# Kernel tuning notes

Measured on AMD Instinct MI355X. Metric: run time of the kernel, lower is better.

## Reference

```python
import math
import jax, jax.numpy as jnp
import numpy as np

B, L, C, H = 2, 2048, 1024, 16
D = C // H


def new_gelu(x):
    return 0.5 * x * (1.0 + jnp.tanh(math.sqrt(2.0 / math.pi) * (x + 0.044715 * x ** 3)))


def layer_norm(x, w, b, eps=1e-5):
    mu = jnp.mean(x, axis=-1, keepdims=True)
    var = jnp.var(x, axis=-1, keepdims=True)
    return (x - mu) * jax.lax.rsqrt(var + eps) * w + b


def setup_inputs() -> dict:
    key = jax.random.key(0)
    ks = jax.random.split(key, 8)
    s = 0.02
    return {
        "x": jax.random.normal(ks[0], (B, L, C), dtype=jnp.float32),
        "ln1_w": jnp.ones((C,), jnp.float32),
        "ln1_b": jnp.zeros((C,), jnp.float32),
        "w_attn": jax.random.normal(ks[1], (C, 3 * C), dtype=jnp.float32) * s,
        "b_attn": jnp.zeros((3 * C,), jnp.float32),
        "w_proj": jax.random.normal(ks[2], (C, C), dtype=jnp.float32) * s,
        "b_proj": jnp.zeros((C,), jnp.float32),
        "ln2_w": jnp.ones((C,), jnp.float32),
        "ln2_b": jnp.zeros((C,), jnp.float32),
        "w_fc": jax.random.normal(ks[3], (C, 4 * C), dtype=jnp.float32) * s,
        "b_fc": jnp.zeros((4 * C,), jnp.float32),
        "w_fc2": jax.random.normal(ks[4], (4 * C, C), dtype=jnp.float32) * s,
        "b_fc2": jnp.zeros((C,), jnp.float32),
    }


def reference(x, ln1_w, ln1_b, w_attn, b_attn, w_proj, b_proj,
              ln2_w, ln2_b, w_fc, b_fc, w_fc2, b_fc2):
    # --- self-attention sublayer (pre-LN) ---
    h = layer_norm(x, ln1_w, ln1_b)
    qkv = h @ w_attn + b_attn                              # [B, L, 3C]
    q, k, v = jnp.split(qkv, 3, axis=-1)
    q = q.reshape(B, L, H, D)
    k = k.reshape(B, L, H, D)
    v = v.reshape(B, L, H, D)
    att = jnp.einsum("bqhd,bkhd->bhqk", q, k) * (1.0 / math.sqrt(D))
    causal = jnp.tril(jnp.ones((L, L), dtype=bool))
    att = jnp.where(causal[None, None], att, -jnp.inf)
    att = jax.nn.softmax(att, axis=-1)
    y = jnp.einsum("bhqk,bkhd->bqhd", att, v).reshape(B, L, C)
    y = y @ w_proj + b_proj
    x = x + y
    # --- MLP sublayer (pre-LN) ---
    h = layer_norm(x, ln2_w, ln2_b)
    h = new_gelu(h @ w_fc + b_fc)
    h = h @ w_fc2 + b_fc2
    return x + h
```

## Files before the change

### kernel.cpp

```cpp
#include <hip/hip_runtime.h>
#include <math.h>

#define B_ 2
#define L_ 2048
#define C_ 1024
#define H_ 16
#define M_ (B_*L_)

typedef short s16x8 __attribute__((ext_vector_type(8)));
typedef float f32x4 __attribute__((ext_vector_type(4)));

__device__ __forceinline__ unsigned short f2bf(float f) {
    unsigned int u = __float_as_uint(f);
    u += 0x7fffu + ((u >> 16) & 1u);
    return (unsigned short)(u >> 16);
}

__device__ __forceinline__ void gl_lds16(const void* g, void* l) {
    __builtin_amdgcn_global_load_lds(
        (const __attribute__((address_space(1))) void*)g,
        (__attribute__((address_space(3))) void*)l, 16, 0, 0);
}

__device__ __forceinline__ void ln_row(const float* __restrict__ x,
                                       const float* __restrict__ w,
                                       const float* __restrict__ b,
                                       unsigned short* __restrict__ out,
                                       int row, int t,
                                       float* red0, float* red1, float* mv) {
    float4 v = ((const float4*)(x + (size_t)row * C_))[t];
    float s  = v.x + v.y + v.z + v.w;
    float s2 = v.x*v.x + v.y*v.y + v.z*v.z + v.w*v.w;
    #pragma unroll
    for (int off = 32; off > 0; off >>= 1) {
        s  += __shfl_down(s, off);
        s2 += __shfl_down(s2, off);
    }
    int wave = t >> 6, lane = t & 63;
    if (lane == 0) { red0[wave] = s; red1[wave] = s2; }
    __syncthreads();
    if (t == 0) {
        float a = red0[0] + red0[1] + red0[2] + red0[3];
        float c = red1[0] + red1[1] + red1[2] + red1[3];
        float mean = a * (1.0f / C_);
        mv[0] = mean;
        mv[1] = rsqrtf(c * (1.0f / C_) - mean * mean + 1e-5f);
    }
    __syncthreads();
    float mean = mv[0], rstd = mv[1];
    float4 wv = ((const float4*)w)[t];
    float4 bv = ((const float4*)b)[t];
    ushort4 o;
    o.x = f2bf((v.x - mean) * rstd * wv.x + bv.x);
    o.y = f2bf((v.y - mean) * rstd * wv.y + bv.y);
    o.z = f2bf((v.z - mean) * rstd * wv.z + bv.z);
    o.w = f2bf((v.w - mean) * rstd * wv.w + bv.w);
    *(ushort4*)&out[(size_t)row * C_ + t * 4] = o;
}

__global__ __launch_bounds__(256) void ln_bf16(const float* __restrict__ x,
                                               const float* __restrict__ w,
                                               const float* __restrict__ b,
                                               unsigned short* __restrict__ out) {
    __shared__ float red0[4], red1[4], mv[2];
    ln_row(x, w, b, out, blockIdx.x, threadIdx.x, red0, red1, mv);
}

__global__ __launch_bounds__(256) void prep_kernel(
    const float* __restrict__ W0, unsigned short* __restrict__ T0,
    const float* __restrict__ W1, unsigned short* __restrict__ T1,
    const float* __restrict__ W2, unsigned short* __restrict__ T2,
    const float* __restrict__ W3, unsigned short* __restrict__ T3,
    const float* __restrict__ x, const float* __restrict__ lnw,
    const float* __restrict__ lnb, unsigned short* __restrict__ h) {
    __shared__ unsigned short Ts[32][33];
    __shared__ float red0[4], red1[4], mv[2];
    int id = blockIdx.x;
    int t = threadIdx.x;
    if (id >= 12288) {
        ln_row(x, lnw, lnb, h, id - 12288, t, red0, red1, mv);
        return;
    }
    const float* W; unsigned short* WT; int R, C, bx, by;
    if (id < 3072)      { W = W0; WT = T0; R = 1024; C = 3072; bx = id % 96;  by = id / 96; }
    else if (id < 4096) { W = W1; WT = T1; R = 1024; C = 1024; id -= 3072; bx = id & 31;  by = id >> 5; }
    else if (id < 8192) { W = W2; WT = T2; R = 1024; C = 4096; id -= 4096; bx = id & 127; by = id >> 7; }
    else                { W = W3; WT = T3; R = 4096; C = 1024; id -= 8192; bx = id & 31;  by = id >> 5; }
    int tx = t & 31, ty = t >> 5;
    int c0 = bx * 32, r0 = by * 32;
    #pragma unroll
    for (int k = 0; k < 4; ++k)
        Ts[ty + 8*k][tx] = f2bf(W[(size_t)(r0 + ty + 8*k) * C + c0 + tx]);
    __syncthreads();
    #pragma unroll
    for (int k = 0; k < 4; ++k)
        WT[(size_t)(c0 + ty + 8*k) * R + r0 + tx] = Ts[tx][ty + 8*k];
}

__global__ __launch_bounds__(256) void transpose_v(const unsigned short* __restrict__ qkv,
                                                   unsigned short* __restrict__ Vt) {
    __shared__ unsigned short Ts[32][33];
    int t = threadIdx.x;
    int tx = t & 31, ty = t >> 5;
    int by = blockIdx.y;
    int bh = by >> 1, dt = by & 1;
    int b = bh >> 4, h = bh & 15;
    int l0 = blockIdx.x * 32, d0 = dt * 32;
    #pragma unroll
    for (int k = 0; k < 4; ++k)
        Ts[ty + 8*k][tx] = qkv[(size_t)(b * L_ + l0 + ty + 8*k) * (3*C_) + 2*C_ + h*64 + d0 + tx];
    __syncthreads();
    #pragma unroll
    for (int k = 0; k < 4; ++k)
        Vt[(size_t)(bh*64 + d0 + ty + 8*k) * L_ + l0 + tx] = Ts[tx][ty + 8*k];
}

__device__ __forceinline__ float gelu_f(float x) {
    float u2 = 1.5957691216057308f * (x + 0.044715f * x * x * x);
    return x / (1.0f + __expf(-u2));
}

template<int ACT, int OBF, int TN, int SC, int KS>
__global__ __launch_bounds__(256) void bgemm(const unsigned short* __restrict__ A,
                                             const unsigned short* __restrict__ BT,
                                             const float* __restrict__ bias,
                                             const float* __restrict__ res,
                                             void* __restrict__ Cout,
                                             int M, int N, int K) {
    __shared__ __align__(16) unsigned short As[128 * 64];
    __shared__ __align__(16) unsigned short Bs[TN * 64];
    const int t = threadIdx.x, w = t >> 6, quad = (t & 63) >> 4, ln15 = t & 15;
    constexpr int FJ = TN / 32;
    const int woff_m = (w >> 1) * 64, woff_n = (w & 1) * (TN / 2);
    const int m0g = blockIdx.y * 128, n0g = blockIdx.x * TN;
    f32x4 acc[4][FJ];
    #pragma unroll
    for (int fi = 0; fi < 4; ++fi)
        #pragma unroll
        for (int fj = 0; fj < FJ; ++fj)
            #pragma unroll
            for (int i = 0; i < 4; ++i) acc[fi][fj][i] = 0.0f;

    const int kbeg = (KS > 1) ? (int)blockIdx.z * (K / KS) : 0;
    const int kiters = ((KS > 1) ? K / KS : K) >> 6;

    const unsigned short* ap[4];
    #pragma unroll
    for (int j = 0; j < 4; ++j) {
        int c = j * 256 + t, row = c >> 3, u = (c & 7) ^ (row & 7);
        ap[j] = A + (size_t)(m0g + row) * K + kbeg + u * 8;
    }
    const unsigned short* bp[FJ];
    #pragma unroll
    for (int j = 0; j < FJ; ++j) {
        int c = j * 256 + t, row = c >> 3, u = (c & 7) ^ (row & 7);
        bp[j] = BT + (size_t)(n0g + row) * K + kbeg + u * 8;
    }

    for (int kk = 0; kk < kiters; ++kk) {
        __syncthreads();
        #pragma unroll
        for (int j = 0; j < 4; ++j) {
            gl_lds16(ap[j], As + (j * 256 + w * 64) * 8);
            ap[j] += 64;
        }
        #pragma unroll
        for (int j = 0; j < FJ; ++j) {
            gl_lds16(bp[j], Bs + (j * 256 + w * 64) * 8);
            bp[j] += 64;
        }
        __syncthreads();
        #pragma unroll
        for (int s = 0; s < 2; ++s) {
            s16x8 af[4], bfr[FJ];
            #pragma unroll
            for (int f = 0; f < 4; ++f) {
                int row = woff_m + f * 16 + ln15;
                af[f] = *(const s16x8*)&As[(row * 8 + ((s * 4 + quad) ^ (row & 7))) * 8];
            }
            #pragma unroll
            for (int f = 0; f < FJ; ++f) {
                int row = woff_n + f * 16 + ln15;
                bfr[f] = *(const s16x8*)&Bs[(row * 8 + ((s * 4 + quad) ^ (row & 7))) * 8];
            }
            #pragma unroll
            for (int fi = 0; fi < 4; ++fi)
                #pragma unroll
                for (int fj = 0; fj < FJ; ++fj)
                    acc[fi][fj] = __builtin_amdgcn_mfma_f32_16x16x32_bf16(af[fi], bfr[fj], acc[fi][fj], 0, 0, 0);
        }
    }

    const int colb = n0g + woff_n + ln15;
    if (KS > 1) {
        float* P = (float*)Cout + (size_t)blockIdx.z * M * N;
        #pragma unroll
        for (int fj = 0; fj < FJ; ++fj) {
            const int col = colb + fj * 16;
            #pragma unroll
            for (int fi = 0; fi < 4; ++fi) {
                const int row0 = m0g + woff_m + fi * 16 + quad * 4;
                #pragma unroll
                for (int i = 0; i < 4; ++i)
                    P[(size_t)(row0 + i) * N + col] = acc[fi][fj][i];
            }
        }
        return;
    }
    #pragma unroll
    for (int fj = 0; fj < FJ; ++fj) {
        const int col = colb + fj * 16;
        const float bv = bias[col];
        const float sc = (SC && col < C_) ? 0.125f : 1.0f;
        #pragma unroll
        for (int fi = 0; fi < 4; ++fi) {
            const int row0 = m0g + woff_m + fi * 16 + quad * 4;
            #pragma unroll
            for (int i = 0; i < 4; ++i) {
                float v = acc[fi][fj][i] + bv;
                if (ACT) v = gelu_f(v);
                if (SC) v *= sc;
                size_t off = (size_t)(row0 + i) * N + col;
                if (res != nullptr) v += res[off];
                if (OBF) ((unsigned short*)Cout)[off] = f2bf(v);
                else     ((float*)Cout)[off] = v;
            }
        }
    }
}

__global__ __launch_bounds__(256) void combine_out(const float* __restrict__ p,
                                                   const float* __restrict__ bias,
                                                   const float* __restrict__ res,
                                                   float* __restrict__ out) {
    int idx = blockIdx.x * 256 + threadIdx.x;
    size_t off = (size_t)idx * 4;
    float4 a = *(const float4*)&p[off];
    float4 b = *(const float4*)&p[(size_t)M_ * C_ + off];
    float4 r = *(const float4*)&res[off];
    float4 bb = *(const float4*)&bias[off & (C_ - 1)];
    float4 o;
    o.x = a.x + b.x + r.x + bb.x;
    o.y = a.y + b.y + r.y + bb.y;
    o.z = a.z + b.z + r.z + bb.z;
    o.w = a.w + b.w + r.w + bb.w;
    *(float4*)&out[off] = o;
}

__global__ __launch_bounds__(256) void attn_kernel(const unsigned short* __restrict__ qkv,
                                                   const unsigned short* __restrict__ Vt,
                                                   unsigned short* __restrict__ y) {
    __shared__ __align__(16) unsigned short Qs[64 * 64];
    __shared__ __align__(16) unsigned short Ks[128 * 64];
    __shared__ __align__(16) unsigned short Vs[64 * 128];
    const int t = threadIdx.x, w = t >> 6, quad = (t & 63) >> 4, ln15 = t & 15;
    const int wq = w >> 1, wk = w & 1;
    const int bh = blockIdx.y, b = bh >> 4, h = bh & 15;

    #pragma unroll 1
    for (int rep = 0; rep < 2; ++rep) {
        const int qt = rep == 0 ? (31 - (int)blockIdx.x) : (int)blockIdx.x;
        const int q0 = qt * 64;
        if (rep) __syncthreads();
        #pragma unroll
        for (int j = 0; j < 2; ++j) {
            int c = j * 256 + t;
            int row = c >> 3, u = (c & 7) ^ (row & 7);
            gl_lds16(qkv + (size_t)(b * L_ + q0 + row) * (3*C_) + h * 64 + u * 8,
                     Qs + (j * 256 + w * 64) * 8);
        }
        __syncthreads();
        s16x8 qb[2][2];
        #pragma unroll
        for (int qf = 0; qf < 2; ++qf) {
            int row = wq * 32 + qf * 16 + ln15;
            #pragma unroll
            for (int s = 0; s < 2; ++s)
                qb[qf][s] = *(const s16x8*)&Qs[row * 64 + (((s * 4 + quad)) ^ (row & 7)) * 8];
        }

        f32x4 O[4][2];
        float m_[2] = {-INFINITY, -INFINITY}, l_[2] = {0.0f, 0.0f};
        #pragma unroll
        for (int df = 0; df < 4; ++df)
            #pragma unroll
            for (int qf = 0; qf < 2; ++qf)
                #pragma unroll
                for (int i = 0; i < 4; ++i) O[df][qf][i] = 0.0f;

        const int nkt = (qt >> 1) + 1;
        for (int kt = 0; kt < nkt; ++kt) {
            __syncthreads();
            #pragma unroll
            for (int j = 0; j < 4; ++j) {
                int c = j * 256 + t;
                int row = c >> 3, u = (c & 7) ^ (row & 7);
                gl_lds16(qkv + (size_t)(b * L_ + kt * 128 + row) * (3*C_) + C_ + h * 64 + u * 8,
                         Ks + (j * 256 + w * 64) * 8);
            }
            #pragma unroll
            for (int j = 0; j < 4; ++j) {
                int c = j * 256 + t;
                int row = c >> 4, u = (c & 15) ^ (row & 15);
                gl_lds16(Vt + (size_t)(bh * 64 + row) * L_ + kt * 128 + u * 8,
                         Vs + (j * 256 + w * 64) * 8);
            }
            __syncthreads();

            f32x4 St[2][4];
            #pragma unroll
            for (int qf = 0; qf < 2; ++qf)
                #pragma unroll
                for (int kf = 0; kf < 4; ++kf)
                    #pragma unroll
                    for (int i = 0; i < 4; ++i) St[qf][kf][i] = 0.0f;
            #pragma unroll
            for (int s = 0; s < 2; ++s) {
                s16x8 ka[4];
                #pragma unroll
                for (int kf = 0; kf < 4; ++kf) {
                    int row = wk * 64 + kf * 16 + ln15;
                    ka[kf] = *(const s16x8*)&Ks[row * 64 + ((s * 4 + quad) ^ (row & 7)) * 8];
                }
                #pragma unroll
                for (int qf = 0; qf < 2; ++qf)
                    #pragma unroll
                    for (int kf = 0; kf < 4; ++kf)
                        St[qf][kf] = __builtin_amdgcn_mfma_f32_16x16x32_bf16(ka[kf], qb[qf][s], St[qf][kf], 0, 0, 0);
            }
            __syncthreads();

            unsigned short* Pw = Ks + w * 2048;
            const bool diag = (kt == nkt - 1);
            #pragma unroll
            for (int qf = 0; qf < 2; ++qf) {
                const int qg = q0 + wq * 32 + qf * 16 + ln15;
                float mt = -INFINITY;
                if (diag) {
                    #pragma unroll
                    for (int kf = 0; kf < 4; ++kf)
                        #pragma unroll
                        for (int i = 0; i < 4; ++i) {
                            int key = kt * 128 + wk * 64 + kf * 16 + quad * 4 + i;
                            float sv = St[qf][kf][i];
                            sv = (key > qg) ? -INFINITY : sv;
                            St[qf][kf][i] = sv;
                            mt = fmaxf(mt, sv);
                        }
                } else {
                    #pragma unroll
                    for (int kf = 0; kf < 4; ++kf)
                        #pragma unroll
                        for (int i = 0; i < 4; ++i) mt = fmaxf(mt, St[qf][kf][i]);
                }
                mt = fmaxf(mt, __shfl_xor(mt, 16));
                mt = fmaxf(mt, __shfl_xor(mt, 32));
                const float mn = fmaxf(m_[qf], mt);
                const float ms = (mn == -INFINITY) ? 0.0f : mn;
                const float alpha = __expf(m_[qf] - ms);
                float rs = 0.0f;
                #pragma unroll
                for (int kf = 0; kf < 4; ++kf)
                    #pragma unroll
                    for (int i = 0; i < 4; ++i) {
                        float e = __expf(St[qf][kf][i] - ms);
                        St[qf][kf][i] = e;
                        rs += e;
                    }
                rs += __shfl_xor(rs, 16);
                rs += __shfl_xor(rs, 32);
                l_[qf] = l_[qf] * alpha + rs;
                m_[qf] = mn;
                #pragma unroll
                for (int df = 0; df < 4; ++df) O[df][qf] *= alpha;
                #pragma unroll
                for (int kf = 0; kf < 4; ++kf) {
                    int row = qf * 16 + ln15;
                    int slot = (kf * 2 + (quad >> 1)) ^ (row & 7);
                    unsigned u0 = __float_as_uint(St[qf][kf][0]) + 0x8000u;
                    unsigned u1 = __float_as_uint(St[qf][kf][1]) + 0x8000u;
                    unsigned u2 = __float_as_uint(St[qf][kf][2]) + 0x8000u;
                    unsigned u3 = __float_as_uint(St[qf][kf][3]) + 0x8000u;
                    uint2 pk;
                    pk.x = __builtin_amdgcn_perm(u1, u0, 0x07060302u);
                    pk.y = __builtin_amdgcn_perm(u3, u2, 0x07060302u);
                    *(uint2*)&Pw[row * 64 + slot * 8 + (quad & 1) * 4] = pk;
                }
            }

            #pragma unroll
            for (int s2 = 0; s2 < 2; ++s2) {
                s16x8 pb[2], va[4];
                #pragma unroll
                for (int qf = 0; qf < 2; ++qf) {
                    int row = qf * 16 + ln15;
                    pb[qf] = *(const s16x8*)&Pw[row * 64 + ((s2 * 4 + quad) ^ (row & 7)) * 8];
                }
                #pragma unroll
                for (int df = 0; df < 4; ++df) {
                    int row = df * 16 + ln15;
                    int uu = wk * 8 + s2 * 4 + quad;
                    va[df] = *(const s16x8*)&Vs[row * 128 + (uu ^ (row & 15)) * 8];
                }
                #pragma unroll
                for (int df = 0; df < 4; ++df)
                    #pragma unroll
                    for (int qf = 0; qf < 2; ++qf)
                        O[df][qf] = __builtin_amdgcn_mfma_f32_16x16x32_bf16(va[df], pb[qf], O[df][qf], 0, 0, 0);
            }
        }

        __syncthreads();
        float* OB  = (float*)Vs;
        float* MLm = (float*)Qs;
        float* MLl = MLm + 64;
        if (wk == 1) {
            #pragma unroll
            for (int qf = 0; qf < 2; ++qf) {
                int rq = wq * 32 + qf * 16 + ln15;
                if (quad == 0) { MLm[rq] = m_[qf]; MLl[rq] = l_[qf]; }
                #pragma unroll
                for (int df = 0; df < 4; ++df) {
                    float4 o;
                    o.x = O[df][qf][0]; o.y = O[df][qf][1]; o.z = O[df][qf][2]; o.w = O[df][qf][3];
                    *(float4*)&OB[rq * 64 + df * 16 + quad * 4] = o;
                }
            }
        }
        __syncthreads();
        if (wk == 0) {
            #pragma unroll
            for (int qf = 0; qf < 2; ++qf) {
                const int rq = wq * 32 + qf * 16 + ln15;
                const float m1 = MLm[rq], l1 = MLl[rq];
                const float mF = fmaxf(m_[qf], m1);
                float e0 = __expf(m_[qf] - mF);
                float e1 = (m1 == -INFINITY) ? 0.0f : __expf(m1 - mF);
                const float linv = 1.0f / (l_[qf] * e0 + l1 * e1);
                e0 *= linv; e1 *= linv;
                #pragma unroll
                for (int df = 0; df < 4; ++df) {
                    float4 o1 = *(const float4*)&OB[rq * 64 + df * 16 + quad * 4];
                    ushort4 yv;
                    yv.x = f2bf(O[df][qf][0] * e0 + o1.x * e1);
                    yv.y = f2bf(O[df][qf][1] * e0 + o1.y * e1);
                    yv.z = f2bf(O[df][qf][2] * e0 + o1.z * e1);
                    yv.w = f2bf(O[df][qf][3] * e0 + o1.w * e1);
                    *(ushort4*)&y[(size_t)(b * L_ + q0 + rq) * C_ + h * 64 + df * 16 + quad * 4] = yv;
                }
            }
        }
    }
}

#define MB(x) ((size_t)(x) << 20)

extern "C" void kernel_launch(void* const* d_in, const int* in_sizes, int n_in,
                              void* d_out, int out_size, void* d_ws, size_t ws_size,
                              hipStream_t stream) {
    const float* x      = (const float*)d_in[0];
    const float* ln1_w  = (const float*)d_in[1];
    const float* ln1_b  = (const float*)d_in[2];
    const float* w_attn = (const float*)d_in[3];
    const float* b_attn = (const float*)d_in[4];
    const float* w_proj = (const float*)d_in[5];
    const float* b_proj = (const float*)d_in[6];
    const float* ln2_w  = (const float*)d_in[7];
    const float* ln2_b  = (const float*)d_in[8];
    const float* w_fc   = (const float*)d_in[9];
    const float* b_fc   = (const float*)d_in[10];
    const float* w_fc2  = (const float*)d_in[11];
    const float* b_fc2  = (const float*)d_in[12];
    float* out = (float*)d_out;

    char* ws = (char*)d_ws;
    unsigned short* wT1  = (unsigned short*)(ws + MB(0));
    unsigned short* wT2  = (unsigned short*)(ws + MB(6));
    unsigned short* wT3  = (unsigned short*)(ws + MB(8));
    unsigned short* wT4  = (unsigned short*)(ws + MB(16));
    unsigned short* h_bf = (unsigned short*)(ws + MB(24));
    unsigned short* qkv  = (unsigned short*)(ws + MB(32));
    unsigned short* Vt   = (unsigned short*)(ws + MB(56));
    unsigned short* y_bf = (unsigned short*)(ws + MB(64));
    float*          x1   = (float*)(ws + MB(72));
    unsigned short* f_bf = (unsigned short*)(ws + MB(88));
    float*          part = (float*)(ws + MB(32));
    dim3 b256(256);

    prep_kernel<<<12288 + M_, b256, 0, stream>>>(w_attn, wT1, w_proj, wT2,
                                                 w_fc, wT3, w_fc2, wT4,
                                                 x, ln1_w, ln1_b, h_bf);
    bgemm<0,1,128,1,1><<<dim3(3*C_/128, M_/128), b256, 0, stream>>>(h_bf, wT1, b_attn, nullptr, qkv, M_, 3*C_, C_);
    transpose_v<<<dim3(L_/32, B_*H_*2), b256, 0, stream>>>(qkv, Vt);
    attn_kernel<<<dim3(L_/128, B_*H_), b256, 0, stream>>>(qkv, Vt, y_bf);
    bgemm<0,0,64,0,1><<<dim3(C_/64, M_/128), b256, 0, stream>>>(y_bf, wT2, b_proj, x, x1, M_, C_, C_);
    ln_bf16<<<M_, b256, 0, stream>>>(x1, ln2_w, ln2_b, h_bf);
    bgemm<1,1,128,0,1><<<dim3(4*C_/128, M_/128), b256, 0, stream>>>(h_bf, wT3, b_fc, nullptr, f_bf, M_, 4*C_, C_);
    bgemm<0,0,128,0,2><<<dim3(C_/128, M_/128, 2), b256, 0, stream>>>(f_bf, wT4, nullptr, nullptr, part, M_, C_, 4*C_);
    combine_out<<<(M_*C_)/(4*256), b256, 0, stream>>>(part, b_fc2, x1, out);
}
```

Baseline: 367.6 us.

## Fuse V transpose into QKV GEMM epilogue and use exp2-based softmax

```diff
diff --git a/kernel.cpp b/kernel.cpp
--- a/kernel.cpp
+++ b/kernel.cpp
@@ -14,6 +14,22 @@
     unsigned int u = __float_as_uint(f);
     u += 0x7fffu + ((u >> 16) & 1u);
     return (unsigned short)(u >> 16);
+}
+
+__device__ __forceinline__ float fexp2(float x) {
+#if __has_builtin(__builtin_amdgcn_exp2f)
+    return __builtin_amdgcn_exp2f(x);
+#else
+    return exp2f(x);
+#endif
+}
+
+__device__ __forceinline__ float frcp(float x) {
+#if __has_builtin(__builtin_amdgcn_rcpf)
+    return __builtin_amdgcn_rcpf(x);
+#else
+    return 1.0f / x;
+#endif
 }
 
 __device__ __forceinline__ void gl_lds16(const void* g, void* l) {
@@ -97,35 +113,18 @@
         WT[(size_t)(c0 + ty + 8*k) * R + r0 + tx] = Ts[tx][ty + 8*k];
 }
 
-__global__ __launch_bounds__(256) void transpose_v(const unsigned short* __restrict__ qkv,
-                                                   unsigned short* __restrict__ Vt) {
-    __shared__ unsigned short Ts[32][33];
-    int t = threadIdx.x;
-    int tx = t & 31, ty = t >> 5;
-    int by = blockIdx.y;
-    int bh = by >> 1, dt = by & 1;
-    int b = bh >> 4, h = bh & 15;
-    int l0 = blockIdx.x * 32, d0 = dt * 32;
-    #pragma unroll
-    for (int k = 0; k < 4; ++k)
-        Ts[ty + 8*k][tx] = qkv[(size_t)(b * L_ + l0 + ty + 8*k) * (3*C_) + 2*C_ + h*64 + d0 + tx];
-    __syncthreads();
-    #pragma unroll
-    for (int k = 0; k < 4; ++k)
-        Vt[(size_t)(bh*64 + d0 + ty + 8*k) * L_ + l0 + tx] = Ts[tx][ty + 8*k];
-}
-
 __device__ __forceinline__ float gelu_f(float x) {
     float u2 = 1.5957691216057308f * (x + 0.044715f * x * x * x);
-    return x / (1.0f + __expf(-u2));
-}
-
-template<int ACT, int OBF, int TN, int SC, int KS>
+    return x * frcp(1.0f + __expf(-u2));
+}
+
+template<int ACT, int OBF, int TN, int SC, int KS, int VT>
 __global__ __launch_bounds__(256) void bgemm(const unsigned short* __restrict__ A,
                                              const unsigned short* __restrict__ BT,
                                              const float* __restrict__ bias,
                                              const float* __restrict__ res,
                                              void* __restrict__ Cout,
+                                             unsigned short* __restrict__ VtP,
                                              int M, int N, int K) {
     __shared__ __align__(16) unsigned short As[128 * 64];
     __shared__ __align__(16) unsigned short Bs[TN * 64];
@@ -211,19 +210,34 @@
     for (int fj = 0; fj < FJ; ++fj) {
         const int col = colb + fj * 16;
         const float bv = bias[col];
-        const float sc = (SC && col < C_) ? 0.125f : 1.0f;
-        #pragma unroll
-        for (int fi = 0; fi < 4; ++fi) {
-            const int row0 = m0g + woff_m + fi * 16 + quad * 4;
-            #pragma unroll
-            for (int i = 0; i < 4; ++i) {
-                float v = acc[fi][fj][i] + bv;
-                if (ACT) v = gelu_f(v);
-                if (SC) v *= sc;
-                size_t off = (size_t)(row0 + i) * N + col;
-                if (res != nullptr) v += res[off];
-                if (OBF) ((unsigned short*)Cout)[off] = f2bf(v);
-                else     ((float*)Cout)[off] = v;
+        const float sc = (SC && col < C_) ? 0.18033688011112042f : 1.0f;
+        if (VT && col >= 2 * C_) {
+            const int vcol = col - 2 * C_;
+            #pragma unroll
+            for (int fi = 0; fi < 4; ++fi) {
+                const int row0 = m0g + woff_m + fi * 16 + quad * 4;
+                const int bb = row0 >> 11, l = row0 & (L_ - 1);
+                ushort4 pk;
+                pk.x = f2bf(acc[fi][fj][0] + bv);
+                pk.y = f2bf(acc[fi][fj][1] + bv);
+                pk.z = f2bf(acc[fi][fj][2] + bv);
+                pk.w = f2bf(acc[fi][fj][3] + bv);
+                *(ushort4*)&VtP[(size_t)(bb * 1024 + vcol) * L_ + l] = pk;
+            }
+        } else {
+            #pragma unroll
+            for (int fi = 0; fi < 4; ++fi) {
+                const int row0 = m0g + woff_m + fi * 16 + quad * 4;
+                #pragma unroll
+                for (int i = 0; i < 4; ++i) {
+                    float v = acc[fi][fj][i] + bv;
+                    if (ACT) v = gelu_f(v);
+                    if (SC) v *= sc;
+                    size_t off = (size_t)(row0 + i) * N + col;
+                    if (res != nullptr) v += res[off];
+                    if (OBF) ((unsigned short*)Cout)[off] = f2bf(v);
+                    else     ((float*)Cout)[off] = v;
+                }
             }
         }
     }
@@ -357,13 +371,13 @@
                 mt = fmaxf(mt, __shfl_xor(mt, 32));
                 const float mn = fmaxf(m_[qf], mt);
                 const float ms = (mn == -INFINITY) ? 0.0f : mn;
-                const float alpha = __expf(m_[qf] - ms);
+                const float alpha = fexp2(m_[qf] - ms);
                 float rs = 0.0f;
                 #pragma unroll
                 for (int kf = 0; kf < 4; ++kf)
                     #pragma unroll
                     for (int i = 0; i < 4; ++i) {
-                        float e = __expf(St[qf][kf][i] - ms);
+                        float e = fexp2(St[qf][kf][i] - ms);
                         St[qf][kf][i] = e;
                         rs += e;
                     }
@@ -434,9 +448,9 @@
                 const int rq = wq * 32 + qf * 16 + ln15;
                 const float m1 = MLm[rq], l1 = MLl[rq];
                 const float mF = fmaxf(m_[qf], m1);
-                float e0 = __expf(m_[qf] - mF);
-                float e1 = (m1 == -INFINITY) ? 0.0f : __expf(m1 - mF);
-                const float linv = 1.0f / (l_[qf] * e0 + l1 * e1);
+                float e0 = fexp2(m_[qf] - mF);
+                float e1 = (m1 == -INFINITY) ? 0.0f : fexp2(m1 - mF);
+                const float linv = frcp(l_[qf] * e0 + l1 * e1);
                 e0 *= linv; e1 *= linv;
                 #pragma unroll
                 for (int df = 0; df < 4; ++df) {
@@ -490,12 +504,15 @@
     prep_kernel<<<12288 + M_, b256, 0, stream>>>(w_attn, wT1, w_proj, wT2,
                                                  w_fc, wT3, w_fc2, wT4,
                                                  x, ln1_w, ln1_b, h_bf);
-    bgemm<0,1,128,1,1><<<dim3(3*C_/128, M_/128), b256, 0, stream>>>(h_bf, wT1, b_attn, nullptr, qkv, M_, 3*C_, C_);
-    transpose_v<<<dim3(L_/32, B_*H_*2), b256, 0, stream>>>(qkv, Vt);
+    bgemm<0,1,128,1,1,1><<<dim3(3*C_/128, M_/128), b256, 0, stream>>>(
+        h_bf, wT1, b_attn, nullptr, qkv, Vt, M_, 3*C_, C_);
     attn_kernel<<<dim3(L_/128, B_*H_), b256, 0, stream>>>(qkv, Vt, y_bf);
-    bgemm<0,0,64,0,1><<<dim3(C_/64, M_/128), b256, 0, stream>>>(y_bf, wT2, b_proj, x, x1, M_, C_, C_);
+    bgemm<0,0,64,0,1,0><<<dim3(C_/64, M_/128), b256, 0, stream>>>(
+        y_bf, wT2, b_proj, x, x1, nullptr, M_, C_, C_);
     ln_bf16<<<M_, b256, 0, stream>>>(x1, ln2_w, ln2_b, h_bf);
-    bgemm<1,1,128,0,1><<<dim3(4*C_/128, M_/128), b256, 0, stream>>>(h_bf, wT3, b_fc, nullptr, f_bf, M_, 4*C_, C_);
-    bgemm<0,0,128,0,2><<<dim3(C_/128, M_/128, 2), b256, 0, stream>>>(f_bf, wT4, nullptr, nullptr, part, M_, C_, 4*C_);
+    bgemm<1,1,128,0,1,0><<<dim3(4*C_/128, M_/128), b256, 0, stream>>>(
+        h_bf, wT3, b_fc, nullptr, f_bf, nullptr, M_, 4*C_, C_);
+    bgemm<0,0,128,0,2,0><<<dim3(C_/128, M_/128, 2), b256, 0, stream>>>(
+        f_bf, wT4, nullptr, nullptr, part, nullptr, M_, C_, 4*C_);
     combine_out<<<(M_*C_)/(4*256), b256, 0, stream>>>(part, b_fc2, x1, out);
 }
```

Result: no change. 364.1 us (-1.0%).
